# Optimization experiments

Measured on AMD Instinct MI355X. Metric: run time of the kernel, lower is better.

Reference implementation:

```python
import jax, jax.numpy as jnp
import numpy as np

B, IN, H, CTX = 16384, 1024, 1024, 2048


def setup_inputs() -> dict:
    key = jax.random.key(0)
    ks = jax.random.split(key, 20)
    stdv = 1.0 / np.sqrt(H)
    u = lambda k, shape: jax.random.uniform(k, shape, jnp.float32, -stdv, stdv)
    inp = {
        "y": jax.random.normal(ks[0], (B, IN), jnp.float32),
        "ctx": jax.random.normal(ks[1], (B, CTX), jnp.float32),
        "c0": jax.random.normal(ks[2], (B, H), jnp.float32),
        "h0": jax.random.normal(ks[3], (B, H), jnp.float32),
        # Concatenated gate weights in order (i, f, o, c), matching the
        # per-gate matrices Wi..Wc, Ui..Uc, Ci..Cc of the original module.
        "W": u(ks[4], (4 * H, IN)),   # input projections
        "U": u(ks[5], (4 * H, H)),    # hidden projections
        "C": u(ks[6], (4 * H, CTX)),  # context projections
        "b": u(ks[7], (4 * H,)),      # gate biases
    }
    return inp


def reference(y, ctx, c0, h0, W, U, C, b):
    # One fused GEMM per input stream instead of 12 small ones; same math.
    gates = y @ W.T + h0 @ U.T + ctx @ C.T + b  # [B, 4H]
    gi, gf, go, gc = jnp.split(gates, 4, axis=-1)
    i = jax.nn.sigmoid(gi)
    f = jax.nn.sigmoid(gf)
    o = jax.nn.sigmoid(go)
    c_hat = jnp.tanh(gc)
    c = i * c_hat + f * c0
    h = o * jnp.tanh(c)
    return (c, h)
```

## Files before the change

kernel.cpp:

```cpp
#include <hip/hip_runtime.h>
#include <hip/hip_bf16.h>
#include <stdint.h>

typedef __attribute__((ext_vector_type(8))) short short8;
typedef __attribute__((ext_vector_type(8))) unsigned short ushort8;
typedef __attribute__((ext_vector_type(4))) float f32x4;
typedef __attribute__((ext_vector_type(8))) __bf16 bf16x8;

#define GAS __attribute__((address_space(1)))
#define LAS __attribute__((address_space(3)))

static constexpr int Bn = 16384;
static constexpr int Hn = 1024;
static constexpr int KT = 4096;
static constexpr int NT = KT / 64;

#define SBAR()   __builtin_amdgcn_s_barrier()
#define VMCNT(n) asm volatile("s_waitcnt vmcnt(" #n ")" ::: "memory")
#define FENCE()  asm volatile("" ::: "memory")

__device__ __forceinline__ unsigned short f2bf(float f) {
  unsigned u = __builtin_bit_cast(unsigned, f);
  u = (u + 0x7FFFu + ((u >> 16) & 1u)) >> 16;
  return (unsigned short)u;
}

__device__ __forceinline__ float fast_sigm(float x) {
  return __builtin_amdgcn_rcpf(1.f + __expf(-x));
}
__device__ __forceinline__ float fast_tanh(float x) {
  return 1.f - 2.f * __builtin_amdgcn_rcpf(__expf(2.f * x) + 1.f);
}

__global__ __launch_bounds__(256) void cvt_concat_k(
    const float* __restrict__ s0, const float* __restrict__ s1,
    const float* __restrict__ s2, unsigned short* __restrict__ dst,
    long long n8) {
  long long stride = (long long)gridDim.x * blockDim.x;
  for (long long g = (long long)blockIdx.x * blockDim.x + threadIdx.x; g < n8;
       g += stride) {
    long long row = g >> 9;
    int cg = (int)(g & 511) << 3;
    const float* src;
    if (cg < 1024)      src = s0 + row * 1024 + cg;
    else if (cg < 2048) src = s1 + row * 1024 + (cg - 1024);
    else                src = s2 + row * 2048 + (cg - 2048);
    float4 f0 = *(const float4*)src;
    float4 f1 = *(const float4*)(src + 4);
    ushort8 o;
    o[0] = f2bf(f0.x); o[1] = f2bf(f0.y); o[2] = f2bf(f0.z); o[3] = f2bf(f0.w);
    o[4] = f2bf(f1.x); o[5] = f2bf(f1.y); o[6] = f2bf(f1.z); o[7] = f2bf(f1.w);
    *(ushort8*)(dst + (g << 3)) = o;
  }
}

__global__ __launch_bounds__(256) void cvt_pack_w(
    const float* __restrict__ s0, const float* __restrict__ s1,
    const float* __restrict__ s2, unsigned short* __restrict__ dst,
    long long n8) {
  long long stride = (long long)gridDim.x * blockDim.x;
  for (long long g = (long long)blockIdx.x * blockDim.x + threadIdx.x; g < n8;
       g += stride) {
    long long row = g >> 9;
    int cg = (int)(g & 511) << 3;
    const float* src;
    if (cg < 1024)      src = s0 + row * 1024 + cg;
    else if (cg < 2048) src = s1 + row * 1024 + (cg - 1024);
    else                src = s2 + row * 2048 + (cg - 2048);
    float4 f0 = *(const float4*)src;
    float4 f1 = *(const float4*)(src + 4);
    ushort8 o;
    o[0] = f2bf(f0.x); o[1] = f2bf(f0.y); o[2] = f2bf(f0.z); o[3] = f2bf(f0.w);
    o[4] = f2bf(f1.x); o[5] = f2bf(f1.y); o[6] = f2bf(f1.z); o[7] = f2bf(f1.w);
    int cb = (int)(row >> 4), fr = (int)(row & 15);
    int k32 = cg >> 5, ksl = (cg >> 3) & 3;
    long long off = ((long long)k32 * 256 + cb) * 512 + (fr + ksl * 16) * 8;
    *(ushort8*)(dst + off) = o;
  }
}

__global__ __launch_bounds__(512, 2) void lstm_gemm(
    const unsigned short* __restrict__ X, const unsigned short* __restrict__ Wp,
    const float* __restrict__ bias, const float* __restrict__ c0,
    float* __restrict__ out_c, float* __restrict__ out_h) {
  extern __shared__ char smem[];

  int bid = blockIdx.x;
  int swz = (bid & 7) * 128 + (bid >> 3);
  int mblk = swz >> 4, cblk = swz & 15;
  int brow0 = mblk * 256;
  int hcol0 = cblk * 64;

  int tid = threadIdx.x;
  int lane = tid & 63, wid = tid >> 6;
  int wr = wid >> 2, wc = wid & 3;

  const char* Xc = (const char*)X;
  const char* Wpc = (const char*)Wp;

  int rr = tid >> 3;
  uint32_t cbyte = (uint32_t)(((tid & 7) * 16) ^ ((rr & 7) << 4));
  uint32_t aoffj[4];
#pragma unroll
  for (int j = 0; j < 4; ++j)
    aoffj[j] = (uint32_t)(brow0 + j * 64 + rr) * (KT * 2) + cbyte;

  auto stage_A = [&](int tt, int dbuf) {
    int ts = tt < NT ? tt : NT - 1;
#pragma unroll
    for (int j = 0; j < 4; ++j) {
      const char* src = Xc + aoffj[j] + (uint32_t)ts * 128u;
      char* dst = smem + dbuf * 32768 + j * 8192 + wid * 1024;
      __builtin_amdgcn_global_load_lds((const GAS unsigned int*)src,
                                       (LAS unsigned int*)dst, 16, 0, 0);
    }
  };

  int kg = (lane >> 4) << 4;
  int sw = (lane & 7) << 4;
  int koff0 = kg ^ sw;
  int koff1 = (64 + kg) ^ sw;
  int fr = lane & 15;

  const char* bbp[4];
#pragma unroll
  for (int n = 0; n < 4; ++n) {
    int cb = n * 64 + cblk * 4 + wc;
    bbp[n] = Wpc + ((size_t)cb * 64 + lane) * 16;
  }

  f32x4 acc[8][4] = {};
  short8 bfrE[4][2], bfrO[4][2];

  stage_A(0, 0);
  FENCE();
#pragma unroll
  for (int n = 0; n < 4; ++n) {
    bfrE[n][0] = *(const short8*)(bbp[n]);
    bfrE[n][1] = *(const short8*)(bbp[n] + 262144);
  }
  stage_A(1, 1);

  int bufA = 0;

#define TILE(T_, BC, BN)                                                      \
  {                                                                           \
    VMCNT(12);                                                                \
    SBAR();                                                                   \
    int pb = bufA * 32768;                                                    \
    int stg = bufA + 2; if (stg >= 3) stg -= 3;                               \
    _Pragma("unroll")                                                         \
    for (int q = 0; q < 4; ++q) {                                             \
      int ab = pb + ((2 * q + wr) * 32 + fr) * 128;                           \
      short8 a0 = *(const short8*)(smem + ab + koff0);                        \
      short8 a1 = *(const short8*)(smem + ab + koff1);                        \
      short8 a2 = *(const short8*)(smem + ab + 2048 + koff0);                 \
      short8 a3 = *(const short8*)(smem + ab + 2048 + koff1);                 \
      if (q == 1) {          \
        int ts = (T_) + 1 < NT ? (T_) + 1 : NT - 1;                           \
        size_t tb = (size_t)(2 * ts) * 262144u;                               \
        _Pragma("unroll")                                                     \
        for (int n = 0; n < 4; ++n) {                                         \
          BN[n][0] = *(const short8*)(bbp[n] + tb);                           \
          BN[n][1] = *(const short8*)(bbp[n] + tb + 262144);                  \
        }                                                                     \
      }                                                                       \
      if (q == 3) stage_A((T_) + 2, stg);                                     \
      __builtin_amdgcn_s_setprio(1);                                          \
      _Pragma("unroll")                                                       \
      for (int n = 0; n < 4; ++n) {                                           \
        acc[2 * q][n] = __builtin_amdgcn_mfma_f32_16x16x32_bf16(              \
            __builtin_bit_cast(bf16x8, a0), __builtin_bit_cast(bf16x8, BC[n][0]),\
            acc[2 * q][n], 0, 0, 0);                                          \
        acc[2 * q + 1][n] = __builtin_amdgcn_mfma_f32_16x16x32_bf16(          \
            __builtin_bit_cast(bf16x8, a2), __builtin_bit_cast(bf16x8, BC[n][0]),\
            acc[2 * q + 1][n], 0, 0, 0);                                      \
      }                                                                       \
      _Pragma("unroll")                                                       \
      for (int n = 0; n < 4; ++n) {                                           \
        acc[2 * q][n] = __builtin_amdgcn_mfma_f32_16x16x32_bf16(              \
            __builtin_bit_cast(bf16x8, a1), __builtin_bit_cast(bf16x8, BC[n][1]),\
            acc[2 * q][n], 0, 0, 0);                                          \
        acc[2 * q + 1][n] = __builtin_amdgcn_mfma_f32_16x16x32_bf16(          \
            __builtin_bit_cast(bf16x8, a3), __builtin_bit_cast(bf16x8, BC[n][1]),\
            acc[2 * q + 1][n], 0, 0, 0);                                      \
      }                                                                       \
      __builtin_amdgcn_s_setprio(0);                                          \
    }                                                                         \
    bufA = bufA + 1; if (bufA >= 3) bufA = 0;                                 \
  }

  for (int t = 0; t < NT; t += 2) {
    TILE(t, bfrE, bfrO)
    TILE(t + 1, bfrO, bfrE)
  }
#undef TILE

  int col = hcol0 + wc * 16 + fr;
  float bi = bias[col], bf_ = bias[1024 + col];
  float bo = bias[2048 + col], bc = bias[3072 + col];
#pragma unroll
  for (int m = 0; m < 8; ++m) {
    int row0 = brow0 + (2 * (m >> 1) + wr) * 32 + (m & 1) * 16 + ((lane >> 4) << 2);
#pragma unroll
    for (int j = 0; j < 4; ++j) {
      size_t idx = (size_t)(row0 + j) * 1024 + col;
      float i_ = fast_sigm(acc[m][0][j] + bi);
      float f_ = fast_sigm(acc[m][1][j] + bf_);
      float o_ = fast_sigm(acc[m][2][j] + bo);
      float ch = fast_tanh(acc[m][3][j] + bc);
      float cn = i_ * ch + f_ * c0[idx];
      out_c[idx] = cn;
      out_h[idx] = o_ * fast_tanh(cn);
    }
  }
}

__global__ __launch_bounds__(256) void lstm_naive(
    const float* __restrict__ y, const float* __restrict__ ctx,
    const float* __restrict__ c0, const float* __restrict__ h0,
    const float* __restrict__ W, const float* __restrict__ U,
    const float* __restrict__ C, const float* __restrict__ b,
    float* __restrict__ out_c, float* __restrict__ out_h) {
  size_t t = (size_t)blockIdx.x * blockDim.x + threadIdx.x;
  if (t >= (size_t)Bn * Hn) return;
  int row = (int)(t >> 10), col = (int)(t & 1023);
  float g[4];
#pragma unroll
  for (int gg = 0; gg < 4; ++gg) {
    int wrow = gg * 1024 + col;
    float s = b[wrow];
    const float* yr = y + (size_t)row * 1024;
    const float* Wr = W + (size_t)wrow * 1024;
    for (int k = 0; k < 1024; ++k) s += yr[k] * Wr[k];
    const float* hr = h0 + (size_t)row * 1024;
    const float* Ur = U + (size_t)wrow * 1024;
    for (int k = 0; k < 1024; ++k) s += hr[k] * Ur[k];
    const float* cr = ctx + (size_t)row * 2048;
    const float* Cr = C + (size_t)wrow * 2048;
    for (int k = 0; k < 2048; ++k) s += cr[k] * Cr[k];
    g[gg] = s;
  }
  float i_ = fast_sigm(g[0]), f_ = fast_sigm(g[1]);
  float o_ = fast_sigm(g[2]), ch = fast_tanh(g[3]);
  float cn = i_ * ch + f_ * c0[t];
  out_c[t] = cn;
  out_h[t] = o_ * fast_tanh(cn);
}

extern "C" void kernel_launch(void* const* d_in, const int* in_sizes, int n_in,
                              void* d_out, int out_size, void* d_ws, size_t ws_size,
                              hipStream_t stream) {
  const float* y   = (const float*)d_in[0];
  const float* ctx = (const float*)d_in[1];
  const float* c0  = (const float*)d_in[2];
  const float* h0  = (const float*)d_in[3];
  const float* W   = (const float*)d_in[4];
  const float* U   = (const float*)d_in[5];
  const float* C   = (const float*)d_in[6];
  const float* b   = (const float*)d_in[7];
  float* out = (float*)d_out;
  float* out_c = out;
  float* out_h = out + (size_t)Bn * Hn;

  const size_t needX = (size_t)Bn * KT * 2;
  const size_t needW = (size_t)(4 * Hn) * KT * 2;

  if (ws_size >= needX + needW) {
    unsigned short* Xb = (unsigned short*)d_ws;
    unsigned short* Wb = (unsigned short*)((char*)d_ws + needX);
    cvt_concat_k<<<2048, 256, 0, stream>>>(y, h0, ctx, Xb, (long long)Bn * 512);
    cvt_pack_w<<<2048, 256, 0, stream>>>(W, U, C, Wb, (long long)(4 * Hn) * 512);
    (void)hipFuncSetAttribute((const void*)lstm_gemm,
                              hipFuncAttributeMaxDynamicSharedMemorySize, 98304);
    lstm_gemm<<<1024, 512, 98304, stream>>>(Xb, Wb, b, c0, out_c, out_h);
  } else {
    lstm_naive<<<(Bn * Hn + 255) / 256, 256, 0, stream>>>(y, ctx, c0, h0, W, U, C,
                                                          b, out_c, out_h);
  }
}
```

Baseline: 585.6 us.

## Switch GEMM to 32x32x16 MFMA with repacked weight and LDS layouts

Replaces the 16x16x32 bf16 MFMA tiles with 32x32x16 MFMA, which needs fewer instructions and fewer operand reads per FLOP. The weight prepack and the A-tile LDS staging layout are reorganized so each lane's fragment sits contiguously, and the old XOR swizzle is dropped. The epilogue uses lane shuffles to gather the four gate values per column, and half the lanes write c while the other half write h. Risks include LDS bank conflicts from the unswizzled layout, higher accumulator register pressure, and redundant c0 loads and activation work in the epilogue.

```diff
diff --git a/kernel.cpp b/kernel.cpp
--- a/kernel.cpp
+++ b/kernel.cpp
@@ -4,7 +4,7 @@
 
 typedef __attribute__((ext_vector_type(8))) short short8;
 typedef __attribute__((ext_vector_type(8))) unsigned short ushort8;
-typedef __attribute__((ext_vector_type(4))) float f32x4;
+typedef __attribute__((ext_vector_type(16))) float f32x16;
 typedef __attribute__((ext_vector_type(8))) __bf16 bf16x8;
 
 #define GAS __attribute__((address_space(1)))
@@ -57,25 +57,26 @@
 __global__ __launch_bounds__(256) void cvt_pack_w(
     const float* __restrict__ s0, const float* __restrict__ s1,
     const float* __restrict__ s2, unsigned short* __restrict__ dst,
-    long long n8) {
+    long long ntot) {
   long long stride = (long long)gridDim.x * blockDim.x;
-  for (long long g = (long long)blockIdx.x * blockDim.x + threadIdx.x; g < n8;
+  for (long long g = (long long)blockIdx.x * blockDim.x + threadIdx.x; g < ntot;
        g += stride) {
-    long long row = g >> 9;
-    int cg = (int)(g & 511) << 3;
+    int l = (int)(g & 63);
+    int gf = (int)((g >> 6) & 127);
+    int k16g = (int)(g >> 13);
+    int gate = ((gf & 1) << 1) | ((l >> 4) & 1);
+    int row = (gate << 10) | ((gf >> 1) << 4) | (l & 15);
+    int k0 = (k16g << 4) + ((l >> 5) << 3);
     const float* src;
-    if (cg < 1024)      src = s0 + row * 1024 + cg;
-    else if (cg < 2048) src = s1 + row * 1024 + (cg - 1024);
-    else                src = s2 + row * 2048 + (cg - 2048);
+    if (k0 < 1024)      src = s0 + (size_t)row * 1024 + k0;
+    else if (k0 < 2048) src = s1 + (size_t)row * 1024 + (k0 - 1024);
+    else                src = s2 + (size_t)row * 2048 + (k0 - 2048);
     float4 f0 = *(const float4*)src;
     float4 f1 = *(const float4*)(src + 4);
     ushort8 o;
     o[0] = f2bf(f0.x); o[1] = f2bf(f0.y); o[2] = f2bf(f0.z); o[3] = f2bf(f0.w);
     o[4] = f2bf(f1.x); o[5] = f2bf(f1.y); o[6] = f2bf(f1.z); o[7] = f2bf(f1.w);
-    int cb = (int)(row >> 4), fr = (int)(row & 15);
-    int k32 = cg >> 5, ksl = (cg >> 3) & 3;
-    long long off = ((long long)k32 * 256 + cb) * 512 + (fr + ksl * 16) * 8;
-    *(ushort8*)(dst + off) = o;
+    *(ushort8*)(dst + (g << 3)) = o;
   }
 }
 
@@ -98,47 +99,44 @@
   const char* Xc = (const char*)X;
   const char* Wpc = (const char*)Wp;
 
-  int rr = tid >> 3;
-  uint32_t cbyte = (uint32_t)(((tid & 7) * 16) ^ ((rr & 7) << 4));
   uint32_t aoffj[4];
 #pragma unroll
-  for (int j = 0; j < 4; ++j)
-    aoffj[j] = (uint32_t)(brow0 + j * 64 + rr) * (KT * 2) + cbyte;
+  for (int j = 0; j < 4; ++j) {
+    int rec = wid * 4 + j;
+    int m32 = rec >> 2, k16 = rec & 3;
+    aoffj[j] = (uint32_t)(brow0 + m32 * 32 + (lane & 31)) * 8192u + k16 * 32 +
+               ((lane >> 5) << 4);
+  }
 
   auto stage_A = [&](int tt, int dbuf) {
     int ts = tt < NT ? tt : NT - 1;
 #pragma unroll
     for (int j = 0; j < 4; ++j) {
       const char* src = Xc + aoffj[j] + (uint32_t)ts * 128u;
-      char* dst = smem + dbuf * 32768 + j * 8192 + wid * 1024;
+      char* dst = smem + dbuf * 32768 + (wid * 4 + j) * 1024;
       __builtin_amdgcn_global_load_lds((const GAS unsigned int*)src,
                                        (LAS unsigned int*)dst, 16, 0, 0);
     }
   };
 
-  int kg = (lane >> 4) << 4;
-  int sw = (lane & 7) << 4;
-  int koff0 = kg ^ sw;
-  int koff1 = (64 + kg) ^ sw;
-  int fr = lane & 15;
-
-  const char* bbp[4];
-#pragma unroll
-  for (int n = 0; n < 4; ++n) {
-    int cb = n * 64 + cblk * 4 + wc;
-    bbp[n] = Wpc + ((size_t)cb * 64 + lane) * 16;
-  }
-
-  f32x4 acc[8][4] = {};
-  short8 bfrE[4][2], bfrO[4][2];
+  const char* bbp[2];
+#pragma unroll
+  for (int s = 0; s < 2; ++s) {
+    int gf = (cblk * 4 + wc) * 2 + s;
+    bbp[s] = Wpc + (size_t)gf * 1024 + (lane << 4);
+  }
+
+  f32x16 acc[4][2] = {};
+  short8 bfrE[2][4], bfrO[2][4];
 
   stage_A(0, 0);
   FENCE();
 #pragma unroll
-  for (int n = 0; n < 4; ++n) {
-    bfrE[n][0] = *(const short8*)(bbp[n]);
-    bfrE[n][1] = *(const short8*)(bbp[n] + 262144);
-  }
+  for (int s = 0; s < 2; ++s)
+#pragma unroll
+    for (int k = 0; k < 4; ++k)
+      bfrE[s][k] = *(const short8*)(bbp[s] + (size_t)k * 131072);
+  FENCE();
   stage_A(1, 1);
 
   int bufA = 0;
@@ -151,39 +149,39 @@
     int stg = bufA + 2; if (stg >= 3) stg -= 3;                               \
     _Pragma("unroll")                                                         \
     for (int q = 0; q < 4; ++q) {                                             \
-      int ab = pb + ((2 * q + wr) * 32 + fr) * 128;                           \
-      short8 a0 = *(const short8*)(smem + ab + koff0);                        \
-      short8 a1 = *(const short8*)(smem + ab + koff1);                        \
-      short8 a2 = *(const short8*)(smem + ab + 2048 + koff0);                 \
-      short8 a3 = *(const short8*)(smem + ab + 2048 + koff1);                 \
+      short8 a0 = *(const short8*)(smem + pb + (((wr * 4 + 0) * 4 + q) << 10) \
+                                   + (lane << 4));                            \
+      short8 a1 = *(const short8*)(smem + pb + (((wr * 4 + 1) * 4 + q) << 10) \
+                                   + (lane << 4));                            \
+      short8 a2 = *(const short8*)(smem + pb + (((wr * 4 + 2) * 4 + q) << 10) \
+                                   + (lane << 4));                            \
+      short8 a3 = *(const short8*)(smem + pb + (((wr * 4 + 3) * 4 + q) << 10) \
+                                   + (lane << 4));                            \
       if (q == 1) {          \
         int ts = (T_) + 1 < NT ? (T_) + 1 : NT - 1;                           \
-        size_t tb = (size_t)(2 * ts) * 262144u;                               \
+        size_t tb = (size_t)(4 * ts) * 131072u;                               \
         _Pragma("unroll")                                                     \
-        for (int n = 0; n < 4; ++n) {                                         \
-          BN[n][0] = *(const short8*)(bbp[n] + tb);                           \
-          BN[n][1] = *(const short8*)(bbp[n] + tb + 262144);                  \
-        }                                                                     \
+        for (int s = 0; s < 2; ++s)                                           \
+          _Pragma("unroll")                                                   \
+          for (int k = 0; k < 4; ++k)                                         \
+            BN[s][k] = *(const short8*)(bbp[s] + tb + (size_t)k * 131072);    \
       }                                                                       \
       if (q == 3) stage_A((T_) + 2, stg);                                     \
       __builtin_amdgcn_s_setprio(1);                                          \
       _Pragma("unroll")                                                       \
-      for (int n = 0; n < 4; ++n) {                                           \
-        acc[2 * q][n] = __builtin_amdgcn_mfma_f32_16x16x32_bf16(              \
-            __builtin_bit_cast(bf16x8, a0), __builtin_bit_cast(bf16x8, BC[n][0]),\
-            acc[2 * q][n], 0, 0, 0);                                          \
-        acc[2 * q + 1][n] = __builtin_amdgcn_mfma_f32_16x16x32_bf16(          \
-            __builtin_bit_cast(bf16x8, a2), __builtin_bit_cast(bf16x8, BC[n][0]),\
-            acc[2 * q + 1][n], 0, 0, 0);                                      \
-      }                                                                       \
-      _Pragma("unroll")                                                       \
-      for (int n = 0; n < 4; ++n) {                                           \
-        acc[2 * q][n] = __builtin_amdgcn_mfma_f32_16x16x32_bf16(              \
-            __builtin_bit_cast(bf16x8, a1), __builtin_bit_cast(bf16x8, BC[n][1]),\
-            acc[2 * q][n], 0, 0, 0);                                          \
-        acc[2 * q + 1][n] = __builtin_amdgcn_mfma_f32_16x16x32_bf16(          \
-            __builtin_bit_cast(bf16x8, a3), __builtin_bit_cast(bf16x8, BC[n][1]),\
-            acc[2 * q + 1][n], 0, 0, 0);                                      \
+      for (int s = 0; s < 2; ++s) {                                           \
+        acc[0][s] = __builtin_amdgcn_mfma_f32_32x32x16_bf16(                  \
+            __builtin_bit_cast(bf16x8, a0), __builtin_bit_cast(bf16x8, BC[s][q]),\
+            acc[0][s], 0, 0, 0);                                              \
+        acc[1][s] = __builtin_amdgcn_mfma_f32_32x32x16_bf16(                  \
+            __builtin_bit_cast(bf16x8, a1), __builtin_bit_cast(bf16x8, BC[s][q]),\
+            acc[1][s], 0, 0, 0);                                              \
+        acc[2][s] = __builtin_amdgcn_mfma_f32_32x32x16_bf16(                  \
+            __builtin_bit_cast(bf16x8, a2), __builtin_bit_cast(bf16x8, BC[s][q]),\
+            acc[2][s], 0, 0, 0);                                              \
+        acc[3][s] = __builtin_amdgcn_mfma_f32_32x32x16_bf16(                  \
+            __builtin_bit_cast(bf16x8, a3), __builtin_bit_cast(bf16x8, BC[s][q]),\
+            acc[3][s], 0, 0, 0);                                              \
       }                                                                       \
       __builtin_amdgcn_s_setprio(0);                                          \
     }                                                                         \
@@ -196,22 +194,31 @@
   }
 #undef TILE
 
-  int col = hcol0 + wc * 16 + fr;
-  float bi = bias[col], bf_ = bias[1024 + col];
-  float bo = bias[2048 + col], bc = bias[3072 + col];
-#pragma unroll
-  for (int m = 0; m < 8; ++m) {
-    int row0 = brow0 + (2 * (m >> 1) + wr) * 32 + (m & 1) * 16 + ((lane >> 4) << 2);
-#pragma unroll
-    for (int j = 0; j < 4; ++j) {
-      size_t idx = (size_t)(row0 + j) * 1024 + col;
-      float i_ = fast_sigm(acc[m][0][j] + bi);
-      float f_ = fast_sigm(acc[m][1][j] + bf_);
-      float o_ = fast_sigm(acc[m][2][j] + bo);
-      float ch = fast_tanh(acc[m][3][j] + bc);
+  int col = hcol0 + wc * 16 + (lane & 15);
+  float b0 = bias[col], b1 = bias[1024 + col];
+  float b2 = bias[2048 + col], b3 = bias[3072 + col];
+  bool hi = (lane & 16) != 0;
+#pragma unroll
+  for (int m = 0; m < 4; ++m) {
+    int rbase = brow0 + (wr * 4 + m) * 32 + ((lane >> 5) << 2);
+#pragma unroll
+    for (int reg = 0; reg < 16; ++reg) {
+      int grow = rbase + (reg & 3) + ((reg >> 2) << 3);
+      size_t idx = (size_t)grow * 1024 + col;
+      float v0 = acc[m][0][reg], v1 = acc[m][1][reg];
+      float x0 = __shfl_xor(v0, 16);
+      float x1 = __shfl_xor(v1, 16);
+      float g0 = hi ? x0 : v0;
+      float g1 = hi ? v0 : x0;
+      float g2 = hi ? x1 : v1;
+      float g3 = hi ? v1 : x1;
+      float i_ = fast_sigm(g0 + b0);
+      float f_ = fast_sigm(g1 + b1);
+      float o_ = fast_sigm(g2 + b2);
+      float ch = fast_tanh(g3 + b3);
       float cn = i_ * ch + f_ * c0[idx];
-      out_c[idx] = cn;
-      out_h[idx] = o_ * fast_tanh(cn);
+      if (!hi) out_c[idx] = cn;
+      else     out_h[idx] = o_ * fast_tanh(cn);
     }
   }
 }
@@ -270,7 +277,7 @@
     unsigned short* Xb = (unsigned short*)d_ws;
     unsigned short* Wb = (unsigned short*)((char*)d_ws + needX);
     cvt_concat_k<<<2048, 256, 0, stream>>>(y, h0, ctx, Xb, (long long)Bn * 512);
-    cvt_pack_w<<<2048, 256, 0, stream>>>(W, U, C, Wb, (long long)(4 * Hn) * 512);
+    cvt_pack_w<<<2048, 256, 0, stream>>>(W, U, C, Wb, (long long)(256 * 128 * 64));
     (void)hipFuncSetAttribute((const void*)lstm_gemm,
                               hipFuncAttributeMaxDynamicSharedMemorySize, 98304);
     lstm_gemm<<<1024, 512, 98304, stream>>>(Xb, Wb, b, c0, out_c, out_h);
```

Result: slower. 749.1 us (+27.9%).
